# Kernel tuning notes

Measured on AMD Instinct MI355X. Metric: run time of the kernel, lower is better.

Reference implementation:

```python
import jax, jax.numpy as jnp
import numpy as np

D_MODEL = 512
NHEAD = 8
D_K = D_MODEL // NHEAD
SCALE = float(np.sqrt(D_K))


def setup_inputs() -> dict:
    key = jax.random.key(0)
    ks = jax.random.split(key, 11)
    B, S = 2, 4096
    std = 1.0 / np.sqrt(D_MODEL)
    inp = {
        'q': jax.random.normal(ks[0], (B, S, D_MODEL), jnp.float32),
        'k': jax.random.normal(ks[1], (B, S, D_MODEL), jnp.float32),
        'v': jax.random.normal(ks[2], (B, S, D_MODEL), jnp.float32),
        'w_q': jax.random.normal(ks[3], (D_MODEL, D_MODEL), jnp.float32) * std,
        'b_q': jax.random.normal(ks[4], (D_MODEL,), jnp.float32) * std,
        'w_k': jax.random.normal(ks[5], (D_MODEL, D_MODEL), jnp.float32) * std,
        'b_k': jax.random.normal(ks[6], (D_MODEL,), jnp.float32) * std,
        'w_v': jax.random.normal(ks[7], (D_MODEL, D_MODEL), jnp.float32) * std,
        'b_v': jax.random.normal(ks[8], (D_MODEL,), jnp.float32) * std,
        'w_o': jax.random.normal(ks[9], (D_MODEL, D_MODEL), jnp.float32) * std,
        'b_o': jax.random.normal(ks[10], (D_MODEL,), jnp.float32) * std,
    }
    return inp


def reference(q, k, v, w_q, b_q, w_k, b_k, w_v, b_v, w_o, b_o):
    B, S, _ = q.shape
    # torch Linear: y = x @ W.T + b
    def proj(x, W, b):
        y = x @ W.T + b
        return y.reshape(B, -1, NHEAD, D_K).transpose(0, 2, 1, 3)  # [B,H,S,Dk]
    qh = proj(q, w_q, b_q)
    kh = proj(k, w_k, b_k)
    vh = proj(v, w_v, b_v)
    scores = jnp.einsum('bhsd,bhtd->bhst', qh, kh) / SCALE  # [B,H,S,S]
    attn = jax.nn.softmax(scores, axis=-1)
    out = jnp.einsum('bhst,bhtd->bhsd', attn, vh)  # [B,H,S,Dk]
    out = out.transpose(0, 2, 1, 3).reshape(B, S, D_MODEL)
    return out @ w_o.T + b_o
```

## Files before the change

kernel.cpp:

```cpp
#include <hip/hip_runtime.h>
#include <stdint.h>

#define DM 512
#define S_LEN 4096
#define NH 8
#define DK 64

typedef __attribute__((ext_vector_type(8))) short bf16x8;
typedef __attribute__((ext_vector_type(4))) float f32x4;

#define QSCALE 0.18033688011112042f
#define NEGBIAS -17.312340490667562f

__device__ inline ushort f2bf(float f) {
  union { float f; uint32_t u; } v; v.f = f;
  uint32_t r = v.u + 0x7fff + ((v.u >> 16) & 1);
  return (ushort)(r >> 16);
}
__device__ inline uint32_t fu(float f) {
  union { float f; uint32_t u; } v; v.f = f; return v.u;
}
__device__ inline uint32_t pktrunc(float lo, float hi) {
  return __builtin_amdgcn_perm(fu(hi), fu(lo), 0x07060302);
}

__device__ inline void async_cp16(const ushort* g, ushort* l) {
  __builtin_amdgcn_global_load_lds((const __attribute__((address_space(1))) void*)g,
                                   (__attribute__((address_space(3))) void*)l, 16, 0, 0);
}

__global__ __launch_bounds__(256) void cvt_all(
    const float4* __restrict__ s0, ushort* __restrict__ d0,
    const float4* __restrict__ s1, ushort* __restrict__ d1,
    const float4* __restrict__ s2, ushort* __restrict__ d2,
    const float4* __restrict__ s3, ushort* __restrict__ d3,
    const float4* __restrict__ x0, ushort* __restrict__ y0,
    const float4* __restrict__ x1, ushort* __restrict__ y1,
    const float4* __restrict__ x2, ushort* __restrict__ y2) {
  if (blockIdx.x < 256) {
    int i = blockIdx.x * 256 + threadIdx.x;
    { float4 v = s0[i]; ushort4 o = {f2bf(v.x), f2bf(v.y), f2bf(v.z), f2bf(v.w)}; *(ushort4*)&d0[i * 4] = o; }
    { float4 v = s1[i]; ushort4 o = {f2bf(v.x), f2bf(v.y), f2bf(v.z), f2bf(v.w)}; *(ushort4*)&d1[i * 4] = o; }
    { float4 v = s2[i]; ushort4 o = {f2bf(v.x), f2bf(v.y), f2bf(v.z), f2bf(v.w)}; *(ushort4*)&d2[i * 4] = o; }
    { float4 v = s3[i]; ushort4 o = {f2bf(v.x), f2bf(v.y), f2bf(v.z), f2bf(v.w)}; *(ushort4*)&d3[i * 4] = o; }
  } else {
    int b = blockIdx.x - 256;
    #pragma unroll
    for (int r = 0; r < 2; r++) {
      int i = (b * 2 + r) * 256 + threadIdx.x;
      { float4 v = x0[i]; ushort4 o = {f2bf(v.x), f2bf(v.y), f2bf(v.z), f2bf(v.w)}; *(ushort4*)&y0[i * 4] = o; }
      { float4 v = x1[i]; ushort4 o = {f2bf(v.x), f2bf(v.y), f2bf(v.z), f2bf(v.w)}; *(ushort4*)&y1[i * 4] = o; }
      { float4 v = x2[i]; ushort4 o = {f2bf(v.x), f2bf(v.y), f2bf(v.z), f2bf(v.w)}; *(ushort4*)&y2[i * 4] = o; }
    }
  }
}

__global__ __launch_bounds__(256) void gemm_proj(
    const ushort* __restrict__ xq, const ushort* __restrict__ xk, const ushort* __restrict__ xv,
    const ushort* __restrict__ wq, const ushort* __restrict__ wk, const ushort* __restrict__ wv,
    const float* __restrict__ bq, const float* __restrict__ bk, const float* __restrict__ bv,
    ushort* __restrict__ Qh, ushort* __restrict__ Kh, ushort* __restrict__ VhT) {
  const ushort* A; const ushort* Bt; const float* bias; float cs;
  if (blockIdx.z == 0)      { A = xq; Bt = wq; bias = bq; cs = QSCALE; }
  else if (blockIdx.z == 1) { A = xk; Bt = wk; bias = bk; cs = 1.0f; }
  else                      { A = xv; Bt = wv; bias = bv; cs = 1.0f; }

  __shared__ ushort As[128 * 32];
  __shared__ ushort Bs[128 * 32];
  const int tid = threadIdx.x;
  const int w = tid >> 6, lane = tid & 63;
  const int quad = lane >> 4, l16 = lane & 15;
  const int wm = w >> 1, wn = w & 1;
  const int m0 = blockIdx.y * 128, n0 = blockIdx.x * 128;
  const f32x4 zero4 = {0.f, 0.f, 0.f, 0.f};

  f32x4 acc[4][4];
  #pragma unroll
  for (int i = 0; i < 4; i++)
    #pragma unroll
    for (int j = 0; j < 4; j++) acc[i][j] = zero4;

  for (int kb = 0; kb < 16; kb++) {
    const int k0 = kb * 32;
    #pragma unroll
    for (int r = 0; r < 2; r++) {
      int idx = r * 256 + tid;
      async_cp16(&A [(size_t)(m0 + (idx >> 2)) * DM + k0 + (idx & 3) * 8], &As[idx * 8]);
      async_cp16(&Bt[(size_t)(n0 + (idx >> 2)) * DM + k0 + (idx & 3) * 8], &Bs[idx * 8]);
    }
    __syncthreads();
    bf16x8 af[4], bfr[4];
    #pragma unroll
    for (int i = 0; i < 4; i++) {
      af[i]  = *(const bf16x8*)&As[(wm * 64 + i * 16 + l16) * 32 + quad * 8];
      bfr[i] = *(const bf16x8*)&Bs[(wn * 64 + i * 16 + l16) * 32 + quad * 8];
    }
    #pragma unroll
    for (int i = 0; i < 4; i++)
      #pragma unroll
      for (int j = 0; j < 4; j++)
        acc[i][j] = __builtin_amdgcn_mfma_f32_16x16x32_bf16(af[i], bfr[j], acc[i][j], 0, 0, 0);
    __syncthreads();
  }

  if (blockIdx.z != 2) {
    ushort* C = (blockIdx.z == 0) ? Qh : Kh;
    #pragma unroll
    for (int j = 0; j < 4; j++) {
      int col_g = n0 + wn * 64 + j * 16 + l16;
      float bv = bias[col_g];
      int h = col_g >> 6, d = col_g & 63;
      #pragma unroll
      for (int i = 0; i < 4; i++) {
        #pragma unroll
        for (int r = 0; r < 4; r++) {
          int row_g = m0 + wm * 64 + i * 16 + quad * 4 + r;
          int b = row_g >> 12, s = row_g & 4095;
          C[(((size_t)(b * NH + h) << 12) + s) * DK + d] = f2bf((acc[i][j][r] + bv) * cs);
        }
      }
    }
  } else {
    #pragma unroll
    for (int j = 0; j < 4; j++) {
      int col_g = n0 + wn * 64 + j * 16 + l16;
      float bv = bias[col_g];
      int h = col_g >> 6, d = col_g & 63;
      #pragma unroll
      for (int i = 0; i < 4; i++) {
        int row0 = m0 + wm * 64 + i * 16 + quad * 4;
        int b = row0 >> 12, s0 = row0 & 4095;
        int sl = s0 & 31;
        int sp = (s0 & ~31) | (((sl >> 2) & 3) << 3) | (((sl >> 4) & 1) << 2);
        ushort4 pk = {f2bf(acc[i][j][0] + bv), f2bf(acc[i][j][1] + bv),
                      f2bf(acc[i][j][2] + bv), f2bf(acc[i][j][3] + bv)};
        *(ushort4*)&VhT[((size_t)(b * NH + h) * DK + d) * S_LEN + sp] = pk;
      }
    }
  }
}

__global__ __launch_bounds__(256) void gemm_out(const ushort* __restrict__ A,
                                                const ushort* __restrict__ Bt,
                                                const float* __restrict__ bias,
                                                float* __restrict__ C) {
  __shared__ ushort As[128 * 32];
  __shared__ ushort Bs[128 * 32];
  const int tid = threadIdx.x;
  const int w = tid >> 6, lane = tid & 63;
  const int quad = lane >> 4, l16 = lane & 15;
  const int wm = w >> 1, wn = w & 1;
  const int m0 = blockIdx.y * 128, n0 = blockIdx.x * 128;
  const f32x4 zero4 = {0.f, 0.f, 0.f, 0.f};

  f32x4 acc[4][4];
  #pragma unroll
  for (int i = 0; i < 4; i++)
    #pragma unroll
    for (int j = 0; j < 4; j++) acc[i][j] = zero4;

  for (int kb = 0; kb < 16; kb++) {
    const int k0 = kb * 32;
    #pragma unroll
    for (int r = 0; r < 2; r++) {
      int idx = r * 256 + tid;
      async_cp16(&A [(size_t)(m0 + (idx >> 2)) * DM + k0 + (idx & 3) * 8], &As[idx * 8]);
      async_cp16(&Bt[(size_t)(n0 + (idx >> 2)) * DM + k0 + (idx & 3) * 8], &Bs[idx * 8]);
    }
    __syncthreads();
    bf16x8 af[4], bfr[4];
    #pragma unroll
    for (int i = 0; i < 4; i++) {
      af[i]  = *(const bf16x8*)&As[(wm * 64 + i * 16 + l16) * 32 + quad * 8];
      bfr[i] = *(const bf16x8*)&Bs[(wn * 64 + i * 16 + l16) * 32 + quad * 8];
    }
    #pragma unroll
    for (int i = 0; i < 4; i++)
      #pragma unroll
      for (int j = 0; j < 4; j++)
        acc[i][j] = __builtin_amdgcn_mfma_f32_16x16x32_bf16(af[i], bfr[j], acc[i][j], 0, 0, 0);
    __syncthreads();
  }

  #pragma unroll
  for (int j = 0; j < 4; j++) {
    int col_g = n0 + wn * 64 + j * 16 + l16;
    float bv = bias[col_g];
    #pragma unroll
    for (int i = 0; i < 4; i++) {
      #pragma unroll
      for (int r = 0; r < 4; r++) {
        int row_g = m0 + wm * 64 + i * 16 + quad * 4 + r;
        C[(size_t)row_g * DM + col_g] = acc[i][j][r] + bv;
      }
    }
  }
}

typedef union { bf16x8 v; uint32_t u[4]; } pfu;

__global__ __launch_bounds__(512, 4) void attn(const ushort* __restrict__ Qh,
                                               const ushort* __restrict__ Kh,
                                               const ushort* __restrict__ VhT,
                                               ushort* __restrict__ O) {
  __shared__ ushort smem[2][16384];
  const int tid = threadIdx.x;
  const int w = tid >> 6, lane = tid & 63;
  const int quad = lane >> 4, l16 = lane & 15;
  const int half = w >> 2;
  const int qw = w & 3;
  const int bh = blockIdx.x;
  const int q0 = blockIdx.y * 128 + qw * 32;
  const size_t base = (size_t)bh * S_LEN * DK;
  const f32x4 zero4 = {0.f, 0.f, 0.f, 0.f};
  const f32x4 negb = {NEGBIAS, NEGBIAS, NEGBIAS, NEGBIAS};
  const short one_bf = (short)0x3F80;
  const bf16x8 ones = {one_bf, one_bf, one_bf, one_bf, one_bf, one_bf, one_bf, one_bf};

  if (blockIdx.y >= 16) {
    #pragma unroll
    for (int i = 0; i < 6; i++) __builtin_amdgcn_s_sleep(7);
  }

  bf16x8 qf[2][2];
  #pragma unroll
  for (int i = 0; i < 2; i++)
    #pragma unroll
    for (int c = 0; c < 2; c++)
      qf[i][c] = *(const bf16x8*)&Qh[base + (size_t)(q0 + i * 16 + l16) * DK + c * 32 + quad * 8];

  f32x4 o[2][4];
  f32x4 l_acc[2];
  #pragma unroll
  for (int i = 0; i < 2; i++) {
    l_acc[i] = zero4;
    #pragma unroll
    for (int n = 0; n < 4; n++) o[i][n] = zero4;
  }

  #define STAGE(IT, BUF) do {                                                         \
    const int t0_ = (IT) * 128;                                                       \
    _Pragma("unroll")                                                                 \
    for (int r_ = 0; r_ < 2; r_++) {                                                  \
      int idx = r_ * 512 + tid;                                                       \
      int row = idx >> 3;                                                             \
      int cl = ((idx & 7) << 4) ^ ((row & 7) << 4);                                   \
      async_cp16(&Kh[base + (size_t)(t0_ + row) * DK + (cl >> 1)], &smem[BUF][idx * 8]); \
    }                                                                                 \
    _Pragma("unroll")                                                                 \
    for (int r_ = 0; r_ < 2; r_++) {                                                  \
      int idx = r_ * 512 + tid;                                                       \
      int row = idx >> 4;                                                             \
      int cl = ((idx & 15) << 4) ^ ((row & 7) << 4);                                  \
      async_cp16(&VhT[base + (size_t)row * S_LEN + t0_ + (cl >> 1)], &smem[BUF][8192 + idx * 8]); \
    }                                                                                 \
  } while (0)

  STAGE(0, 0);
  __syncthreads();

  const int swz = (l16 & 7) << 4;

  for (int it = 0; it < 32; it++) {
    const int cur = it & 1;
    if (it < 31) STAGE(it + 1, cur ^ 1);
    const ushort* Kb = &smem[cur][0];
    const ushort* Vb = &smem[cur][8192];

    bf16x8 kf[4][2];
    #pragma unroll
    for (int s = 0; s < 4; s++) {
      int row = half * 64 + s * 16 + l16;
      kf[s][0] = *(const bf16x8*)&Kb[row * 64 + ((( 0 + quad * 16) ^ swz) >> 1)];
      kf[s][1] = *(const bf16x8*)&Kb[row * 64 + (((64 + quad * 16) ^ swz) >> 1)];
    }
    f32x4 sc[2][4];
    __builtin_amdgcn_s_setprio(1);
    #pragma unroll
    for (int i = 0; i < 2; i++)
      #pragma unroll
      for (int s = 0; s < 4; s++) {
        f32x4 t = negb;
        t = __builtin_amdgcn_mfma_f32_16x16x32_bf16(kf[s][0], qf[i][0], t, 0, 0, 0);
        t = __builtin_amdgcn_mfma_f32_16x16x32_bf16(kf[s][1], qf[i][1], t, 0, 0, 0);
        sc[i][s] = t;
      }
    __builtin_amdgcn_s_setprio(0);
    float p[2][4][4];
    #pragma unroll
    for (int i = 0; i < 2; i++)
      #pragma unroll
      for (int s = 0; s < 4; s++)
        #pragma unroll
        for (int r = 0; r < 4; r++)
          p[i][s][r] = __builtin_amdgcn_exp2f(sc[i][s][r]);
    pfu pf[2][2];
    #pragma unroll
    for (int i = 0; i < 2; i++)
      #pragma unroll
      for (int ppl = 0; ppl < 2; ppl++) {
        int s0 = ppl * 2, s1 = ppl * 2 + 1;
        pf[i][ppl].u[0] = pktrunc(p[i][s0][0], p[i][s0][1]);
        pf[i][ppl].u[1] = pktrunc(p[i][s0][2], p[i][s0][3]);
        pf[i][ppl].u[2] = pktrunc(p[i][s1][0], p[i][s1][1]);
        pf[i][ppl].u[3] = pktrunc(p[i][s1][2], p[i][s1][3]);
        l_acc[i] = __builtin_amdgcn_mfma_f32_16x16x32_bf16(pf[i][ppl].v, ones, l_acc[i], 0, 0, 0);
      }
    bf16x8 vf[4][2];
    #pragma unroll
    for (int n = 0; n < 4; n++) {
      int row = n * 16 + l16;
      #pragma unroll
      for (int ppl = 0; ppl < 2; ppl++)
        vf[n][ppl] = *(const bf16x8*)&Vb[row * 128 + ((((half * 2 + ppl) * 64 + quad * 16) ^ swz) >> 1)];
    }
    __builtin_amdgcn_s_setprio(1);
    #pragma unroll
    for (int n = 0; n < 4; n++)
      #pragma unroll
      for (int ppl = 0; ppl < 2; ppl++)
        #pragma unroll
        for (int i = 0; i < 2; i++)
          o[i][n] = __builtin_amdgcn_mfma_f32_16x16x32_bf16(pf[i][ppl].v, vf[n][ppl], o[i][n], 0, 0, 0);
    __builtin_amdgcn_s_setprio(0);

    __syncthreads();
  }

  float* red = (float*)smem;
  const int roff = (qw * 64 + lane) * 40;
  if (half == 1) {
    #pragma unroll
    for (int i = 0; i < 2; i++) {
      #pragma unroll
      for (int n = 0; n < 4; n++)
        *(f32x4*)&red[roff + (i * 4 + n) * 4] = o[i][n];
      *(f32x4*)&red[roff + 32 + i * 4] = l_acc[i];
    }
  }
  __syncthreads();
  if (half == 0) {
    #pragma unroll
    for (int i = 0; i < 2; i++) {
      #pragma unroll
      for (int n = 0; n < 4; n++)
        o[i][n] += *(const f32x4*)&red[roff + (i * 4 + n) * 4];
      l_acc[i] += *(const f32x4*)&red[roff + 32 + i * 4];
    }
    const int b = bh >> 3, h = bh & 7;
    #pragma unroll
    for (int i = 0; i < 2; i++) {
      #pragma unroll
      for (int r = 0; r < 4; r++) {
        float inv = 1.0f / l_acc[i][r];
        int qq = q0 + i * 16 + quad * 4 + r;
        #pragma unroll
        for (int n = 0; n < 4; n++) {
          int d = n * 16 + l16;
          O[(size_t)(b * S_LEN + qq) * DM + h * DK + d] = f2bf(o[i][n][r] * inv);
        }
      }
    }
  }
}

extern "C" void kernel_launch(void* const* d_in, const int* in_sizes, int n_in,
                              void* d_out, int out_size, void* d_ws, size_t ws_size,
                              hipStream_t stream) {
  const float* q   = (const float*)d_in[0];
  const float* k   = (const float*)d_in[1];
  const float* v   = (const float*)d_in[2];
  const float* w_q = (const float*)d_in[3];
  const float* b_q = (const float*)d_in[4];
  const float* w_k = (const float*)d_in[5];
  const float* b_k = (const float*)d_in[6];
  const float* w_v = (const float*)d_in[7];
  const float* b_v = (const float*)d_in[8];
  const float* w_o = (const float*)d_in[9];
  const float* b_o = (const float*)d_in[10];

  const size_t W_ELEMS = (size_t)DM * DM;
  const size_t X_ELEMS = (size_t)2 * S_LEN * DM;
  const size_t HEADS_ELEMS = (size_t)2 * NH * S_LEN * DK;
  ushort* wqb = (ushort*)d_ws;
  ushort* wkb = wqb + W_ELEMS;
  ushort* wvb = wkb + W_ELEMS;
  ushort* wob = wvb + W_ELEMS;
  ushort* Xq  = wob + W_ELEMS;
  ushort* Xk  = Xq + X_ELEMS;
  ushort* Xv  = Xk + X_ELEMS;
  ushort* Qh  = Xv + X_ELEMS;
  ushort* Kh  = Qh + HEADS_ELEMS;
  ushort* VhT = Kh + HEADS_ELEMS;
  ushort* AttO = VhT + HEADS_ELEMS;

  cvt_all<<<2304, 256, 0, stream>>>((const float4*)w_q, wqb, (const float4*)w_k, wkb,
                                    (const float4*)w_v, wvb, (const float4*)w_o, wob,
                                    (const float4*)q, Xq, (const float4*)k, Xk,
                                    (const float4*)v, Xv);
  gemm_proj<<<dim3(4, 64, 3), 256, 0, stream>>>(Xq, Xk, Xv, wqb, wkb, wvb,
                                                b_q, b_k, b_v, Qh, Kh, VhT);
  attn<<<dim3(16, 32), 512, 0, stream>>>(Qh, Kh, VhT, AttO);
  gemm_out<<<dim3(4, 64), 256, 0, stream>>>(AttO, wob, b_o, (float*)d_out);
}
```

Baseline: 216.4 us.

## Double-buffer LDS tiles in projection and output GEMMs to overlap loads with MFMA

Both GEMM kernels now allocate two shared-memory buffers per operand and prefetch the next K-slice with async copies while MFMAs run on the current one. Previously each iteration waited on its own load before computing. This hides global-to-LDS latency behind compute, at the cost of twice the LDS per block, which may lower occupancy. Correctness depends on async_cp16 completion and the trailing barrier ordering the buffer swaps.

New measurement: 217.3 us. Within noise of the previous version (+0.4%).

```diff
diff --git a/kernel.cpp b/kernel.cpp
--- a/kernel.cpp
+++ b/kernel.cpp
@@ -65,8 +65,8 @@
   else if (blockIdx.z == 1) { A = xk; Bt = wk; bias = bk; cs = 1.0f; }
   else                      { A = xv; Bt = wv; bias = bv; cs = 1.0f; }
 
-  __shared__ ushort As[128 * 32];
-  __shared__ ushort Bs[128 * 32];
+  __shared__ ushort As[2][128 * 32];
+  __shared__ ushort Bs[2][128 * 32];
   const int tid = threadIdx.x;
   const int w = tid >> 6, lane = tid & 63;
   const int quad = lane >> 4, l16 = lane & 15;
@@ -80,20 +80,27 @@
     #pragma unroll
     for (int j = 0; j < 4; j++) acc[i][j] = zero4;
 
+  #define PSTAGE(KB, BUF) do {                                                        \
+    const int k0_ = (KB) * 32;                                                        \
+    _Pragma("unroll")                                                                 \
+    for (int r_ = 0; r_ < 2; r_++) {                                                  \
+      int idx = r_ * 256 + tid;                                                       \
+      async_cp16(&A [(size_t)(m0 + (idx >> 2)) * DM + k0_ + (idx & 3) * 8], &As[BUF][idx * 8]); \
+      async_cp16(&Bt[(size_t)(n0 + (idx >> 2)) * DM + k0_ + (idx & 3) * 8], &Bs[BUF][idx * 8]); \
+    }                                                                                 \
+  } while (0)
+
+  PSTAGE(0, 0);
+  __syncthreads();
+
   for (int kb = 0; kb < 16; kb++) {
-    const int k0 = kb * 32;
-    #pragma unroll
-    for (int r = 0; r < 2; r++) {
-      int idx = r * 256 + tid;
-      async_cp16(&A [(size_t)(m0 + (idx >> 2)) * DM + k0 + (idx & 3) * 8], &As[idx * 8]);
-      async_cp16(&Bt[(size_t)(n0 + (idx >> 2)) * DM + k0 + (idx & 3) * 8], &Bs[idx * 8]);
-    }
-    __syncthreads();
+    const int cur = kb & 1;
+    if (kb < 15) PSTAGE(kb + 1, cur ^ 1);
     bf16x8 af[4], bfr[4];
     #pragma unroll
     for (int i = 0; i < 4; i++) {
-      af[i]  = *(const bf16x8*)&As[(wm * 64 + i * 16 + l16) * 32 + quad * 8];
-      bfr[i] = *(const bf16x8*)&Bs[(wn * 64 + i * 16 + l16) * 32 + quad * 8];
+      af[i]  = *(const bf16x8*)&As[cur][(wm * 64 + i * 16 + l16) * 32 + quad * 8];
+      bfr[i] = *(const bf16x8*)&Bs[cur][(wn * 64 + i * 16 + l16) * 32 + quad * 8];
     }
     #pragma unroll
     for (int i = 0; i < 4; i++)
@@ -144,8 +151,8 @@
                                                 const ushort* __restrict__ Bt,
                                                 const float* __restrict__ bias,
                                                 float* __restrict__ C) {
-  __shared__ ushort As[128 * 32];
-  __shared__ ushort Bs[128 * 32];
+  __shared__ ushort As[2][128 * 32];
+  __shared__ ushort Bs[2][128 * 32];
   const int tid = threadIdx.x;
   const int w = tid >> 6, lane = tid & 63;
   const int quad = lane >> 4, l16 = lane & 15;
@@ -159,20 +166,27 @@
     #pragma unroll
     for (int j = 0; j < 4; j++) acc[i][j] = zero4;
 
+  #define OSTAGE(KB, BUF) do {                                                        \
+    const int k0_ = (KB) * 32;                                                        \
+    _Pragma("unroll")                                                                 \
+    for (int r_ = 0; r_ < 2; r_++) {                                                  \
+      int idx = r_ * 256 + tid;                                                       \
+      async_cp16(&A [(size_t)(m0 + (idx >> 2)) * DM + k0_ + (idx & 3) * 8], &As[BUF][idx * 8]); \
+      async_cp16(&Bt[(size_t)(n0 + (idx >> 2)) * DM + k0_ + (idx & 3) * 8], &Bs[BUF][idx * 8]); \
+    }                                                                                 \
+  } while (0)
+
+  OSTAGE(0, 0);
+  __syncthreads();
+
   for (int kb = 0; kb < 16; kb++) {
-    const int k0 = kb * 32;
-    #pragma unroll
-    for (int r = 0; r < 2; r++) {
-      int idx = r * 256 + tid;
-      async_cp16(&A [(size_t)(m0 + (idx >> 2)) * DM + k0 + (idx & 3) * 8], &As[idx * 8]);
-      async_cp16(&Bt[(size_t)(n0 + (idx >> 2)) * DM + k0 + (idx & 3) * 8], &Bs[idx * 8]);
-    }
-    __syncthreads();
+    const int cur = kb & 1;
+    if (kb < 15) OSTAGE(kb + 1, cur ^ 1);
     bf16x8 af[4], bfr[4];
     #pragma unroll
     for (int i = 0; i < 4; i++) {
-      af[i]  = *(const bf16x8*)&As[(wm * 64 + i * 16 + l16) * 32 + quad * 8];
-      bfr[i] = *(const bf16x8*)&Bs[(wn * 64 + i * 16 + l16) * 32 + quad * 8];
+      af[i]  = *(const bf16x8*)&As[cur][(wm * 64 + i * 16 + l16) * 32 + quad * 8];
+      bfr[i] = *(const bf16x8*)&Bs[cur][(wn * 64 + i * 16 + l16) * 32 + quad * 8];
     }
     #pragma unroll
     for (int i = 0; i < 4; i++)
```
